# Optimization experiments

Measured on AMD Instinct MI355X. Metric: run time of the kernel, lower is better.

## Reference

```python
import jax, jax.numpy as jnp
import numpy as np

B, T, E, H, D = 256, 77, 1280, 20, 64
SCALE = D ** -0.5
NEG = -1e9


def setup_inputs() -> dict:
    key = jax.random.key(0)
    ks = jax.random.split(key, 32)
    w = lambda k, shape, s=0.02: jax.random.normal(k, shape, dtype=jnp.float32) * s
    causal = jnp.triu(jnp.full((T, T), NEG, dtype=jnp.float32), k=1)
    causal_mask = jnp.broadcast_to(causal[None, None], (B, 1, T, T))
    return {
        'hidden_states': jax.random.normal(ks[0], (B, T, E), dtype=jnp.float32),
        'embeds': jax.random.normal(ks[1], (B, T, E), dtype=jnp.float32),
        'causal_mask': causal_mask,
        'q_w': w(ks[2], (E, E)), 'q_b': w(ks[3], (E,)),
        'k_w': w(ks[4], (E, E)), 'k_b': w(ks[5], (E,)),
        'v_w': w(ks[6], (E, E)), 'v_b': w(ks[7], (E,)),
        'o_w': w(ks[8], (E, E)), 'o_b': w(ks[9], (E,)),
        'ka_w': w(ks[10], (E, E)) * 0.01, 'ka_b': w(ks[11], (E,)) * 0.001,
        'va_w': w(ks[12], (E, E)) * 0.01, 'va_b': w(ks[13], (E,)) * 0.001,
        'zc1_w': w(ks[14], (E, E)), 'zc1_b': w(ks[15], (E,)),
        'zt1_w': w(ks[16], (T, 2 * T)), 'zt1_b': w(ks[17], (T,)),
        'zc2_w': w(ks[18], (E, E)), 'zc2_b': w(ks[19], (E,)),
        'zt2_w': w(ks[20], (T, T)), 'zt2_b': w(ks[21], (T,)),
    }


def _heads(x):
    # (B, S, E) -> (B, H, S, D)
    return x.reshape(B, -1, H, D).transpose(0, 2, 1, 3)


def _attend(q, k, v, mask=None):
    # q,k,v: (B,H,*,D); returns (B,T,E)
    logits = jnp.einsum('bhtd,bhsd->bhts', q, k)
    if mask is not None:
        logits = logits + mask  # mask: (B,1,T,S)
    probs = jax.nn.softmax(logits, axis=-1)  # dropout p=0 in eval
    ctx = jnp.einsum('bhts,bhsd->bhtd', probs, v)
    return ctx.transpose(0, 2, 1, 3).reshape(B, T, E)


def _zipper(x, zc1_w, zc1_b, zt1_w, zt1_b, zc2_w, zc2_b, zt2_w, zt2_b):
    # token/channel mixer: (B, 2T, E) -> (B, T, E)
    x = jax.nn.gelu(x @ zc1_w.T + zc1_b)              # channel: E -> hidden E
    x = jnp.swapaxes(x, 1, 2)                          # (B, E, 2T)
    x = jax.nn.gelu(x @ zt1_w.T + zt1_b)               # tokens: 2T -> T
    x = jnp.swapaxes(x, 1, 2)                          # (B, T, E)
    x = x @ zc2_w.T + zc2_b                            # channel: E -> E
    x = jnp.swapaxes(x, 1, 2) @ zt2_w.T + zt2_b        # tokens: T -> T
    return jnp.swapaxes(x, 1, 2)


def reference(hidden_states, embeds, causal_mask,
              q_w, q_b, k_w, k_b, v_w, v_b, o_w, o_b,
              ka_w, ka_b, va_w, va_b,
              zc1_w, zc1_b, zt1_w, zt1_b, zc2_w, zc2_b, zt2_w, zt2_b):
    q = _heads((hidden_states @ q_w.T + q_b) * SCALE)
    k = _heads(hidden_states @ k_w.T + k_b)
    v = _heads(hidden_states @ v_w.T + v_b)
    attn_output = _attend(q, k, v, causal_mask)  # self-attention pass

    # adapter cross-attention pass (shared query)
    ka = _heads(embeds @ ka_w.T + ka_b)
    va = _heads(embeds @ va_w.T + va_b)
    attn_output_adapter = _attend(q, ka, va, None)

    zipped = _zipper(jnp.concatenate([attn_output_adapter, attn_output], axis=1),
                     zc1_w, zc1_b, zt1_w, zt1_b, zc2_w, zc2_b, zt2_w, zt2_b)
    attn_output = attn_output + zipped
    return attn_output @ o_w.T + o_b
```

## Files before the change

kernel.cpp:

```cpp
#include <hip/hip_runtime.h>
#include <stdint.h>

#define B_    256
#define T_    77
#define E_    1280
#define H_    20
#define T2_   154
#define MTOK  19712
#define MTOK2 39424

typedef float f32x4 __attribute__((ext_vector_type(4)));
typedef short bf16x8 __attribute__((ext_vector_type(8)));

__device__ inline float bf2f(short s) {
    return __uint_as_float(((unsigned)(unsigned short)s) << 16);
}
__device__ inline short f2bf(float f) {
    unsigned u = __float_as_uint(f);
    u += 0x7fff + ((u >> 16) & 1);
    return (short)(u >> 16);
}
__device__ inline float gelu_tanh(float x) {
    float x3 = x * x * x;
    return 0.5f * x * (1.0f + tanhf(0.7978845608028654f * (x + 0.044715f * x3)));
}

__global__ void cast_f32_bf16(const float* __restrict__ in, short* __restrict__ out, int n4) {
    int i = blockIdx.x * blockDim.x + threadIdx.x;
    int stride = gridDim.x * blockDim.x;
    for (; i < n4; i += stride) {
        float4 v = reinterpret_cast<const float4*>(in)[i];
        short4 o;
        o.x = f2bf(v.x); o.y = f2bf(v.y); o.z = f2bf(v.z); o.w = f2bf(v.w);
        reinterpret_cast<short4*>(out)[i] = o;
    }
}

__global__ void cast8_f32_bf16(const float* __restrict__ s0, const float* __restrict__ s1,
                               const float* __restrict__ s2, const float* __restrict__ s3,
                               const float* __restrict__ s4, const float* __restrict__ s5,
                               const float* __restrict__ s6, const float* __restrict__ s7,
                               short* __restrict__ out) {
    const int per = E_ * E_ / 4;
    int i = blockIdx.x * blockDim.x + threadIdx.x;
    int stride = gridDim.x * blockDim.x;
    for (; i < 8 * per; i += stride) {
        int w = i / per, j = i - w * per;
        const float* src = w == 0 ? s0 : w == 1 ? s1 : w == 2 ? s2 : w == 3 ? s3
                         : w == 4 ? s4 : w == 5 ? s5 : w == 6 ? s6 : s7;
        float4 v = reinterpret_cast<const float4*>(src)[j];
        short4 o;
        o.x = f2bf(v.x); o.y = f2bf(v.y); o.z = f2bf(v.z); o.w = f2bf(v.w);
        reinterpret_cast<short4*>(out)[i] = o;
    }
}

__global__ void pad_weight(const float* __restrict__ W, short* __restrict__ Wp,
                           int rows, int cols, int KP) {
    int i = blockIdx.x * 256 + threadIdx.x;
    if (i >= 80 * KP) return;
    int t = i / KP, s = i - t * KP;
    Wp[i] = (t < rows && s < cols) ? f2bf(W[t * cols + s]) : (short)0;
}

#define GEMM_CORE(A_, W_, KDIM, ACC)                                                   \
    const int rsub = lane >> 3;                                                        \
    const int col  = (((lane & 7) ^ rsub) & 7) * 8;                                    \
    const int swz  = (lane & 7) << 3;                                                  \
    for (int kt = 0; kt < (KDIM); kt += 64) {                                          \
        __syncthreads();                                                               \
        _Pragma("unroll")                                                              \
        for (int i = 0; i < 4; ++i) {                                                  \
            int chunk = i * 4 + wave;                                                  \
            int row = chunk * 8 + rsub;                                                \
            const short* ga = (A_) + (arow0 + row) * (KDIM) + kt + col;                \
            const short* gb = (W_) + (brow0 + row) * (KDIM) + kt + col;                \
            __builtin_amdgcn_global_load_lds(                                          \
                (const __attribute__((address_space(1))) unsigned int*)ga,             \
                (__attribute__((address_space(3))) unsigned int*)&Als[chunk * 512],    \
                16, 0, 0);                                                             \
            __builtin_amdgcn_global_load_lds(                                          \
                (const __attribute__((address_space(1))) unsigned int*)gb,             \
                (__attribute__((address_space(3))) unsigned int*)&Bls[chunk * 512],    \
                16, 0, 0);                                                             \
        }                                                                              \
        __syncthreads();                                                               \
        _Pragma("unroll")                                                              \
        for (int kk = 0; kk < 2; ++kk) {                                               \
            bf16x8 af[4], bfr[4];                                                      \
            _Pragma("unroll")                                                          \
            for (int mi = 0; mi < 4; ++mi)                                             \
                af[mi] = *reinterpret_cast<const bf16x8*>(                             \
                    &Als[(((wm + mi * 16 + (lane & 15)) * 64 + kk * 32 +               \
                           (lane >> 4) * 8)) ^ swz]);                                  \
            _Pragma("unroll")                                                          \
            for (int nj = 0; nj < 4; ++nj)                                             \
                bfr[nj] = *reinterpret_cast<const bf16x8*>(                            \
                    &Bls[(((wn + nj * 16 + (lane & 15)) * 64 + kk * 32 +               \
                           (lane >> 4) * 8)) ^ swz]);                                  \
            _Pragma("unroll")                                                          \
            for (int mi = 0; mi < 4; ++mi)                                             \
                _Pragma("unroll")                                                      \
                for (int nj = 0; nj < 4; ++nj)                                         \
                    ACC[mi][nj] = __builtin_amdgcn_mfma_f32_16x16x32_bf16(             \
                        af[mi], bfr[nj], ACC[mi][nj], 0, 0, 0);                        \
        }                                                                              \
    }

template<int EPI>
__global__ void gemm_bt(const short* __restrict__ A, const short* __restrict__ W,
                        const float* __restrict__ bias, void* __restrict__ Cout,
                        int K) {
    const int N = E_;
    const int NBN = E_ / 128;
    __shared__ short Als[128 * 64];
    __shared__ short Bls[128 * 64];
    const int tid  = threadIdx.x;
    const int wave = tid >> 6, lane = tid & 63;

    const int nwg = gridDim.x;
    const int qq = nwg >> 3, rr = nwg & 7;
    const int x = blockIdx.x & 7, ii = blockIdx.x >> 3;
    const int L = (x < rr ? x * (qq + 1) : rr * (qq + 1) + (x - rr) * qq) + ii;
    const int bm = L / NBN, bn = L % NBN;

    const int wm = (wave >> 1) * 64, wn = (wave & 1) * 64;
    f32x4 acc[4][4] = {};
    const long arow0 = (long)bm * 128;
    const long brow0 = (long)bn * 128;

    GEMM_CORE(A, W, K, acc)

#pragma unroll
    for (int mi = 0; mi < 4; ++mi) {
#pragma unroll
        for (int nj = 0; nj < 4; ++nj) {
            int gcol = bn * 128 + wn + nj * 16 + (lane & 15);
            float bv = bias[gcol];
#pragma unroll
            for (int r = 0; r < 4; ++r) {
                long grow = arow0 + wm + mi * 16 + (lane >> 4) * 4 + r;
                float v = acc[mi][nj][r] + bv;
                if (EPI == 2) v = gelu_tanh(v);
                if (EPI == 3) ((float*)Cout)[grow * N + gcol] = v;
                else          ((short*)Cout)[grow * N + gcol] = f2bf(v);
            }
        }
    }
}

template<int NSEG>
__global__ void gemm_proj(const short* __restrict__ A, const short* __restrict__ W,
                          const float* __restrict__ b0, const float* __restrict__ b1,
                          const float* __restrict__ b2,
                          short* __restrict__ o0, short* __restrict__ o1,
                          short* __restrict__ o2, float s0) {
    const int PB = (MTOK / 128) * (E_ / 128);
    __shared__ short Als[128 * 64];
    __shared__ short Bls[128 * 64];
    const int tid  = threadIdx.x;
    const int wave = tid >> 6, lane = tid & 63;

    const int nwg = gridDim.x;
    const int qq = nwg >> 3, rr = nwg & 7;
    const int x = blockIdx.x & 7, ii = blockIdx.x >> 3;
    const int L = (x < rr ? x * (qq + 1) : rr * (qq + 1) + (x - rr) * qq) + ii;
    const int seg = L / PB;
    const int rem = L - seg * PB;
    const int bm = rem / (E_ / 128), bnl = rem % (E_ / 128);

    const int wm = (wave >> 1) * 64, wn = (wave & 1) * 64;
    f32x4 acc[4][4] = {};
    const long arow0 = (long)bm * 128;
    const long brow0 = (long)seg * E_ + bnl * 128;
    const int K = E_;

    GEMM_CORE(A, W, K, acc)

    const float* bias = seg == 0 ? b0 : (seg == 1 ? b1 : b2);
    short* out = seg == 0 ? o0 : (seg == 1 ? o1 : o2);
    const float scl = seg == 0 ? s0 : 1.f;
#pragma unroll
    for (int mi = 0; mi < 4; ++mi) {
#pragma unroll
        for (int nj = 0; nj < 4; ++nj) {
            int gcol = bnl * 128 + wn + nj * 16 + (lane & 15);
            float bv = bias[gcol];
#pragma unroll
            for (int r = 0; r < 4; ++r) {
                long grow = arow0 + wm + mi * 16 + (lane >> 4) * 4 + r;
                out[grow * E_ + gcol] = f2bf((acc[mi][nj][r] + bv) * scl);
            }
        }
    }
}

template<int SIN, int KP, int PS, bool GELU, bool RESID>
__global__ void mixer_mfma(const short* __restrict__ IN, const short* __restrict__ Wp,
                           const float* __restrict__ bias, const short* __restrict__ Cat,
                           short* __restrict__ OUT) {
    __shared__ short lsT[64 * PS];
    const int e0 = blockIdx.x * 64;
    const int b  = blockIdx.y;
    const int tid = threadIdx.x, wave = tid >> 6, lane = tid & 63;

    const int eg = tid & 7;
    const int sl = tid >> 3;
    for (int sb = sl; sb < KP; sb += 32) {
        if (sb < SIN) {
            bf16x8 v = *reinterpret_cast<const bf16x8*>(
                &IN[((long)b * SIN + sb) * E_ + e0 + eg * 8]);
#pragma unroll
            for (int i = 0; i < 8; ++i)
                lsT[(eg * 8 + i) * PS + sb] = v[i];
        } else {
#pragma unroll
            for (int i = 0; i < 8; ++i)
                lsT[(eg * 8 + i) * PS + sb] = 0;
        }
    }
    __syncthreads();

    const int ebase = wave * 16;
    f32x4 acc[5] = {};
#pragma unroll
    for (int ks = 0; ks < KP / 32; ++ks) {
        bf16x8 bfr = *reinterpret_cast<const bf16x8*>(
            &lsT[(ebase + (lane & 15)) * PS + ks * 32 + (lane >> 4) * 8]);
#pragma unroll
        for (int mt = 0; mt < 5; ++mt) {
            bf16x8 af = *reinterpret_cast<const bf16x8*>(
                &Wp[(mt * 16 + (lane & 15)) * KP + ks * 32 + (lane >> 4) * 8]);
            acc[mt] = __builtin_amdgcn_mfma_f32_16x16x32_bf16(af, bfr, acc[mt], 0, 0, 0);
        }
    }

    const int e = e0 + ebase + (lane & 15);
#pragma unroll
    for (int mt = 0; mt < 5; ++mt) {
#pragma unroll
        for (int r = 0; r < 4; ++r) {
            int t = mt * 16 + (lane >> 4) * 4 + r;
            if (t < T_) {
                float v = acc[mt][r] + bias[t];
                if (GELU) v = gelu_tanh(v);
                if (RESID) v += bf2f(Cat[((long)b * T2_ + T_ + t) * E_ + e]);
                OUT[((long)b * T_ + t) * E_ + e] = f2bf(v);
            }
        }
    }
}

#define ASTR 104
__global__ __launch_bounds__(64, 1)
void attn_mfma(const short* __restrict__ Qm,
               const short* __restrict__ Km, const short* __restrict__ Vm,
               const short* __restrict__ KAm, const short* __restrict__ VAm,
               short* __restrict__ Cat) {
    __shared__ short pls[80 * ASTR];
    __shared__ short vt[64 * ASTR];
    const int hh = blockIdx.x;
    const int b = hh / H_, h = hh % H_;
    const int lane = threadIdx.x & 63;
    const int colbase = lane & 15, g = lane >> 4;
    const long base = ((long)b * T_) * E_ + h * 64;

    for (int pass = 0; pass < 2; ++pass) {
        const short* Kp = pass ? KAm : Km;
        const short* Vp = pass ? VAm : Vm;
        const bool causal = (pass == 0);
        const int rowoff = pass ? 0 : T_;

        {
            int4 z = {0, 0, 0, 0};
#pragma unroll
            for (int it = 0; it < 4; ++it) {
                int idx = it * 64 + lane;
                int row = idx >> 2, cb = idx & 3;
                *reinterpret_cast<int4*>(&vt[row * ASTR + 64 + cb * 8]) = z;
            }
#pragma unroll
            for (int it = 0; it < 3; ++it) {
                int idx = it * 64 + lane;
                if (idx < 160) {
                    int row = idx >> 1, cb = idx & 1;
                    *reinterpret_cast<int4*>(&pls[row * ASTR + 80 + cb * 8]) = z;
                }
            }
        }

        {
            const short* vb = Vp + base + (long)lane * E_;
#pragma unroll
            for (int dg = 0; dg < 8; ++dg) {
                bf16x8 v = *reinterpret_cast<const bf16x8*>(vb + dg * 8);
#pragma unroll
                for (int i = 0; i < 8; ++i) vt[(dg * 8 + i) * ASTR + lane] = v[i];
            }
            if (lane < T_ - 64) {
                const short* vb2 = Vp + base + (long)(64 + lane) * E_;
#pragma unroll
                for (int dg = 0; dg < 8; ++dg) {
                    bf16x8 v = *reinterpret_cast<const bf16x8*>(vb2 + dg * 8);
#pragma unroll
                    for (int i = 0; i < 8; ++i) vt[(dg * 8 + i) * ASTR + 64 + lane] = v[i];
                }
            }
        }

        f32x4 sacc[5][5] = {};
#pragma unroll
        for (int kk = 0; kk < 2; ++kk) {
            bf16x8 qf[5];
#pragma unroll
            for (int mi = 0; mi < 5; ++mi) {
                int t = mi * 16 + colbase; t = t > 76 ? 76 : t;
                qf[mi] = *reinterpret_cast<const bf16x8*>(
                    Qm + base + (long)t * E_ + kk * 32 + g * 8);
            }
#pragma unroll
            for (int nj = 0; nj < 5; ++nj) {
                int s = nj * 16 + colbase; s = s > 76 ? 76 : s;
                bf16x8 kf = *reinterpret_cast<const bf16x8*>(
                    Kp + base + (long)s * E_ + kk * 32 + g * 8);
#pragma unroll
                for (int mi = 0; mi < 5; ++mi)
                    sacc[mi][nj] = __builtin_amdgcn_mfma_f32_16x16x32_bf16(
                        qf[mi], kf, sacc[mi][nj], 0, 0, 0);
            }
        }

        float inv[5][4];
#pragma unroll
        for (int mi = 0; mi < 5; ++mi) {
#pragma unroll
            for (int r = 0; r < 4; ++r) {
                int t = mi * 16 + g * 4 + r;
                float mx = -3.0e38f;
#pragma unroll
                for (int nj = 0; nj < 5; ++nj) {
                    int s = nj * 16 + colbase;
                    bool ok = causal ? (s <= t) : (s < T_);
                    if (ok) mx = fmaxf(mx, sacc[mi][nj][r]);
                }
#pragma unroll
                for (int o = 1; o <= 8; o <<= 1) mx = fmaxf(mx, __shfl_xor(mx, o));
                float sum = 0.f;
#pragma unroll
                for (int nj = 0; nj < 5; ++nj) {
                    int s = nj * 16 + colbase;
                    bool ok = causal ? (s <= t) : (s < T_);
                    float pv = ok ? __expf(sacc[mi][nj][r] - mx) : 0.f;
                    sacc[mi][nj][r] = pv;
                    sum += pv;
                }
#pragma unroll
                for (int o = 1; o <= 8; o <<= 1) sum += __shfl_xor(sum, o);
                inv[mi][r] = 1.0f / sum;
            }
        }

#pragma unroll
        for (int mi = 0; mi < 5; ++mi)
#pragma unroll
            for (int nj = 0; nj < 5; ++nj)
#pragma unroll
                for (int r = 0; r < 4; ++r)
                    pls[(mi * 16 + g * 4 + r) * ASTR + nj * 16 + colbase] =
                        f2bf(sacc[mi][nj][r]);

        f32x4 cacc[5][4] = {};
#pragma unroll
        for (int ks = 0; ks < 3; ++ks) {
            bf16x8 pa[5];
#pragma unroll
            for (int mi = 0; mi < 5; ++mi)
                pa[mi] = *reinterpret_cast<const bf16x8*>(
                    &pls[(mi * 16 + colbase) * ASTR + ks * 32 + g * 8]);
#pragma unroll
            for (int nd = 0; nd < 4; ++nd) {
                bf16x8 vf = *reinterpret_cast<const bf16x8*>(
                    &vt[(nd * 16 + colbase) * ASTR + ks * 32 + g * 8]);
#pragma unroll
                for (int mi = 0; mi < 5; ++mi)
                    cacc[mi][nd] = __builtin_amdgcn_mfma_f32_16x16x32_bf16(
                        pa[mi], vf, cacc[mi][nd], 0, 0, 0);
            }
        }

#pragma unroll
        for (int mi = 0; mi < 5; ++mi)
#pragma unroll
            for (int nd = 0; nd < 4; ++nd)
#pragma unroll
                for (int r = 0; r < 4; ++r) {
                    int t = mi * 16 + g * 4 + r;
                    if (t < T_) {
                        float val = cacc[mi][nd][r] * inv[mi][r];
                        Cat[((long)b * T2_ + rowoff + t) * E_ + h * 64 + nd * 16 + colbase] =
                            f2bf(val);
                    }
                }
    }
}

extern "C" void kernel_launch(void* const* d_in, const int* in_sizes, int n_in,
                              void* d_out, int out_size, void* d_ws, size_t ws_size,
                              hipStream_t stream) {
    const float* hidden = (const float*)d_in[0];
    const float* embeds = (const float*)d_in[1];
    const float* q_w  = (const float*)d_in[3];  const float* q_b  = (const float*)d_in[4];
    const float* k_w  = (const float*)d_in[5];  const float* k_b  = (const float*)d_in[6];
    const float* v_w  = (const float*)d_in[7];  const float* v_b  = (const float*)d_in[8];
    const float* o_w  = (const float*)d_in[9];  const float* o_b  = (const float*)d_in[10];
    const float* ka_w = (const float*)d_in[11]; const float* ka_b = (const float*)d_in[12];
    const float* va_w = (const float*)d_in[13]; const float* va_b = (const float*)d_in[14];
    const float* zc1_w = (const float*)d_in[15]; const float* zc1_b = (const float*)d_in[16];
    const float* zt1_w = (const float*)d_in[17]; const float* zt1_b = (const float*)d_in[18];
    const float* zc2_w = (const float*)d_in[19]; const float* zc2_b = (const float*)d_in[20];
    const float* zt2_w = (const float*)d_in[21]; const float* zt2_b = (const float*)d_in[22];

    char* ws = (char*)d_ws;
    const size_t WSZ = (size_t)E_ * E_ * 2;
    const size_t ASZ = (size_t)MTOK * E_ * 2;
    short* Wq  = (short*)(ws + 0 * WSZ);
    short* Wka = (short*)(ws + 3 * WSZ);
    short* Wz1 = (short*)(ws + 5 * WSZ);
    short* Wz2 = (short*)(ws + 6 * WSZ);
    short* Wo  = (short*)(ws + 7 * WSZ);
    char* p = ws + 8 * WSZ;
    short* Ahs  = (short*)p; p += ASZ;
    short* Aemb = (short*)p; p += ASZ;
    short* Qb   = (short*)p; p += ASZ;
    short* Kb   = (short*)p; p += ASZ;
    short* Vb   = (short*)p; p += ASZ;
    short* KAb  = (short*)p; p += ASZ;
    short* VAb  = (short*)p; p += ASZ;
    short* Wz1p = (short*)p; p += 80 * 160 * 2;
    short* Wz2p = (short*)p; p += 80 * 96 * 2;
    short* CAT = Ahs;
    short* Y   = KAb;
    short* X2  = Qb;
    short* X3  = Kb;
    short* S   = Vb;

    if (ws_size < (size_t)(p - ws)) return;

    cast_f32_bf16<<<2048, 256, 0, stream>>>(hidden, Ahs,  MTOK * E_ / 4);
    cast_f32_bf16<<<2048, 256, 0, stream>>>(embeds, Aemb, MTOK * E_ / 4);
    cast8_f32_bf16<<<2048, 256, 0, stream>>>(q_w, k_w, v_w, ka_w, va_w, zc1_w, zc2_w, o_w,
                                             Wq);
    pad_weight<<<(80 * 160 + 255) / 256, 256, 0, stream>>>(zt1_w, Wz1p, 77, 154, 160);
    pad_weight<<<(80 * 96 + 255) / 256, 256, 0, stream>>>(zt2_w, Wz2p, 77, 77, 96);

    const int gQKV  = (MTOK / 128) * (3 * E_ / 128);
    const int gKAVA = (MTOK / 128) * (2 * E_ / 128);
    const int g154  = (MTOK / 128) * (E_ / 128);
    const int g308  = (MTOK2 / 128) * (E_ / 128);
    gemm_proj<3><<<gQKV, 256, 0, stream>>>(Ahs, Wq, q_b, k_b, v_b,
                                           Qb, Kb, Vb, 0.125f);
    gemm_proj<2><<<gKAVA, 256, 0, stream>>>(Aemb, Wka, ka_b, va_b, nullptr,
                                            KAb, VAb, nullptr, 1.f);
    attn_mfma<<<B_ * H_, 64, 0, stream>>>(Qb, Kb, Vb, KAb, VAb, CAT);
    gemm_bt<2><<<g308, 256, 0, stream>>>(CAT, Wz1, zc1_b, Y, E_);
    mixer_mfma<154, 160, 168, true, false><<<dim3(E_ / 64, B_), 256, 0, stream>>>(
        Y, Wz1p, zt1_b, nullptr, X2);
    gemm_bt<0><<<g154, 256, 0, stream>>>(X2, Wz2, zc2_b, X3, E_);
    mixer_mfma<77, 96, 104, false, true><<<dim3(E_ / 64, B_), 256, 0, stream>>>(
        X3, Wz2p, zt2_b, CAT, S);
    gemm_bt<3><<<g154, 256, 0, stream>>>(S, Wo, o_b, (float*)d_out, E_);
}
```

Before: 1.057 ms.

## Replace projection and zc1 GEMMs with 256x256 double-buffered 8-wave GEMM kernel

Adds a new qgemm kernel that uses 256x256 output tiles with 512 threads, double-buffered LDS staging through global_load_lds, and a four-phase schedule that interleaves the next tile's loads with MFMA work under explicit waitcnt and barrier control. It replaces the QKV, adapter KA/VA and the zc1 channel GEMMs, which previously used 128x128 single-buffered tiles. The larger tiles are meant to raise data reuse per byte loaded and to hide global memory latency behind compute. In exchange the kernel needs more LDS and registers per block, and the hand-written vmcnt counts make it fragile.

```diff
diff --git a/kernel.cpp b/kernel.cpp
--- a/kernel.cpp
+++ b/kernel.cpp
@@ -61,6 +61,168 @@
     if (i >= 80 * KP) return;
     int t = i / KP, s = i - t * KP;
     Wp[i] = (t < rows && s < cols) ? f2bf(W[t * cols + s]) : (short)0;
+}
+
+template<int NSEG, int EPI>
+__global__ __launch_bounds__(512, 2)
+void qgemm(const short* __restrict__ A, const short* __restrict__ W,
+           const float* __restrict__ b0, const float* __restrict__ b1,
+           const float* __restrict__ b2,
+           short* __restrict__ o0, short* __restrict__ o1, short* __restrict__ o2,
+           float s0) {
+    const int K = E_;
+    const int NT = K / 64;
+    __shared__ short As[2 * 2 * 8192];
+    __shared__ short Bs[2 * 2 * 8192];
+    const int tid = threadIdx.x;
+    const int wave = tid >> 6, lane = tid & 63;
+    const int wr = wave >> 2, wc = wave & 3;
+
+    const int nwg = gridDim.x;
+    const int qq = nwg >> 3, rr = nwg & 7;
+    const int x = blockIdx.x & 7, ii = blockIdx.x >> 3;
+    const int L = (x < rr ? x * (qq + 1) : rr * (qq + 1) + (x - rr) * qq) + ii;
+    const int PB = nwg / NSEG;
+    const int seg = L / PB;
+    const int rem = L - seg * PB;
+    const int bm = rem / 5, bnl = rem % 5;
+
+    const long arow0 = (long)bm * 256;
+    const long brow0 = (long)seg * E_ + bnl * 256;
+
+    const int rsub = lane >> 3;
+    const int colswz = (((lane & 7) ^ rsub) & 7) * 8;
+    const int swz = (lane & 7) << 3;
+
+    f32x4 acc[8][4] = {};
+
+    auto STAGE_A = [&](int par, int half, int kt) {
+#pragma unroll
+        for (int i = 0; i < 2; ++i) {
+            int chunk = i * 8 + wave;
+            int row = chunk * 8 + rsub;
+            const short* ga = A + (arow0 + half * 128 + row) * K + kt * 64 + colswz;
+            __builtin_amdgcn_global_load_lds(
+                (const __attribute__((address_space(1))) unsigned int*)ga,
+                (__attribute__((address_space(3))) unsigned int*)
+                    &As[par * 16384 + half * 8192 + chunk * 512], 16, 0, 0);
+        }
+    };
+    auto STAGE_B = [&](int par, int half, int kt) {
+#pragma unroll
+        for (int i = 0; i < 2; ++i) {
+            int chunk = i * 8 + wave;
+            int row = chunk * 8 + rsub;
+            const short* gb = W + (brow0 + half * 128 + row) * K + kt * 64 + colswz;
+            __builtin_amdgcn_global_load_lds(
+                (const __attribute__((address_space(1))) unsigned int*)gb,
+                (__attribute__((address_space(3))) unsigned int*)
+                    &Bs[par * 16384 + half * 8192 + chunk * 512], 16, 0, 0);
+        }
+    };
+
+    bf16x8 Afr[4][2], Bfr[2][2];
+    auto LDA = [&](int par, int hm) {
+#pragma unroll
+        for (int mi = 0; mi < 4; ++mi)
+#pragma unroll
+            for (int kk = 0; kk < 2; ++kk)
+                Afr[mi][kk] = *reinterpret_cast<const bf16x8*>(
+                    &As[par * 16384 + hm * 8192 +
+                        (((wr * 64 + mi * 16 + (lane & 15)) * 64 + kk * 32 +
+                          (lane >> 4) * 8) ^ swz)]);
+    };
+    auto LDB = [&](int par, int hn) {
+#pragma unroll
+        for (int nj = 0; nj < 2; ++nj)
+#pragma unroll
+            for (int kk = 0; kk < 2; ++kk)
+                Bfr[nj][kk] = *reinterpret_cast<const bf16x8*>(
+                    &Bs[par * 16384 + hn * 8192 +
+                        (((wc * 32 + nj * 16 + (lane & 15)) * 64 + kk * 32 +
+                          (lane >> 4) * 8) ^ swz)]);
+    };
+    auto MFMA16 = [&](int hm, int hn) {
+        __builtin_amdgcn_s_setprio(1);
+#pragma unroll
+        for (int mi = 0; mi < 4; ++mi)
+#pragma unroll
+            for (int nj = 0; nj < 2; ++nj)
+#pragma unroll
+                for (int kk = 0; kk < 2; ++kk)
+                    acc[hm * 4 + mi][hn * 2 + nj] =
+                        __builtin_amdgcn_mfma_f32_16x16x32_bf16(
+                            Afr[mi][kk], Bfr[nj][kk], acc[hm * 4 + mi][hn * 2 + nj],
+                            0, 0, 0);
+        __builtin_amdgcn_s_setprio(0);
+    };
+
+    STAGE_A(0, 0, 0); STAGE_B(0, 0, 0); STAGE_B(0, 1, 0); STAGE_A(0, 1, 0);
+
+    for (int t = 0; t < NT - 1; ++t) {
+        const int par = t & 1, nxt = par ^ 1;
+        asm volatile("s_waitcnt vmcnt(4)" ::: "memory");
+        __builtin_amdgcn_s_barrier(); __builtin_amdgcn_sched_barrier(0);
+        LDA(par, 0); LDB(par, 0);
+        STAGE_A(nxt, 0, t + 1);
+        MFMA16(0, 0);
+        asm volatile("s_waitcnt vmcnt(4)" ::: "memory");
+        __builtin_amdgcn_s_barrier(); __builtin_amdgcn_sched_barrier(0);
+        LDB(par, 1);
+        STAGE_B(nxt, 0, t + 1);
+        MFMA16(0, 1);
+        asm volatile("s_waitcnt vmcnt(4)" ::: "memory");
+        __builtin_amdgcn_s_barrier(); __builtin_amdgcn_sched_barrier(0);
+        LDA(par, 1); LDB(par, 0);
+        STAGE_B(nxt, 1, t + 1);
+        MFMA16(1, 0);
+        __builtin_amdgcn_s_barrier(); __builtin_amdgcn_sched_barrier(0);
+        LDB(par, 1);
+        STAGE_A(nxt, 1, t + 1);
+        MFMA16(1, 1);
+    }
+    {
+        const int par = (NT - 1) & 1;
+        asm volatile("s_waitcnt vmcnt(4)" ::: "memory");
+        __builtin_amdgcn_s_barrier(); __builtin_amdgcn_sched_barrier(0);
+        LDA(par, 0); LDB(par, 0);
+        MFMA16(0, 0);
+        asm volatile("s_waitcnt vmcnt(2)" ::: "memory");
+        __builtin_amdgcn_s_barrier(); __builtin_amdgcn_sched_barrier(0);
+        LDB(par, 1);
+        MFMA16(0, 1);
+        asm volatile("s_waitcnt vmcnt(0)" ::: "memory");
+        __builtin_amdgcn_s_barrier(); __builtin_amdgcn_sched_barrier(0);
+        LDA(par, 1); LDB(par, 0);
+        MFMA16(1, 0);
+        __builtin_amdgcn_s_barrier(); __builtin_amdgcn_sched_barrier(0);
+        LDB(par, 1);
+        MFMA16(1, 1);
+    }
+
+    const float* bias = seg == 0 ? b0 : (seg == 1 ? b1 : b2);
+    short* out = seg == 0 ? o0 : (seg == 1 ? o1 : o2);
+    const float scl = (EPI == 0 && seg == 0) ? s0 : 1.f;
+#pragma unroll
+    for (int hm = 0; hm < 2; ++hm)
+#pragma unroll
+        for (int mi = 0; mi < 4; ++mi)
+#pragma unroll
+            for (int hn = 0; hn < 2; ++hn)
+#pragma unroll
+                for (int nj = 0; nj < 2; ++nj) {
+                    int ncol = bnl * 256 + hn * 128 + wc * 32 + nj * 16 + (lane & 15);
+                    float bv = bias[ncol];
+#pragma unroll
+                    for (int r = 0; r < 4; ++r) {
+                        long grow = arow0 + hm * 128 + wr * 64 + mi * 16 +
+                                    (lane >> 4) * 4 + r;
+                        float v = acc[hm * 4 + mi][hn * 2 + nj][r] + bv;
+                        if (EPI == 2) v = gelu_tanh(v);
+                        else v *= scl;
+                        out[grow * E_ + ncol] = f2bf(v);
+                    }
+                }
 }
 
 #define GEMM_CORE(A_, W_, KDIM, ACC)                                                   \
@@ -141,55 +303,8 @@
             for (int r = 0; r < 4; ++r) {
                 long grow = arow0 + wm + mi * 16 + (lane >> 4) * 4 + r;
                 float v = acc[mi][nj][r] + bv;
-                if (EPI == 2) v = gelu_tanh(v);
                 if (EPI == 3) ((float*)Cout)[grow * N + gcol] = v;
                 else          ((short*)Cout)[grow * N + gcol] = f2bf(v);
-            }
-        }
-    }
-}
-
-template<int NSEG>
-__global__ void gemm_proj(const short* __restrict__ A, const short* __restrict__ W,
-                          const float* __restrict__ b0, const float* __restrict__ b1,
-                          const float* __restrict__ b2,
-                          short* __restrict__ o0, short* __restrict__ o1,
-                          short* __restrict__ o2, float s0) {
-    const int PB = (MTOK / 128) * (E_ / 128);
-    __shared__ short Als[128 * 64];
-    __shared__ short Bls[128 * 64];
-    const int tid  = threadIdx.x;
-    const int wave = tid >> 6, lane = tid & 63;
-
-    const int nwg = gridDim.x;
-    const int qq = nwg >> 3, rr = nwg & 7;
-    const int x = blockIdx.x & 7, ii = blockIdx.x >> 3;
-    const int L = (x < rr ? x * (qq + 1) : rr * (qq + 1) + (x - rr) * qq) + ii;
-    const int seg = L / PB;
-    const int rem = L - seg * PB;
-    const int bm = rem / (E_ / 128), bnl = rem % (E_ / 128);
-
-    const int wm = (wave >> 1) * 64, wn = (wave & 1) * 64;
-    f32x4 acc[4][4] = {};
-    const long arow0 = (long)bm * 128;
-    const long brow0 = (long)seg * E_ + bnl * 128;
-    const int K = E_;
-
-    GEMM_CORE(A, W, K, acc)
-
-    const float* bias = seg == 0 ? b0 : (seg == 1 ? b1 : b2);
-    short* out = seg == 0 ? o0 : (seg == 1 ? o1 : o2);
-    const float scl = seg == 0 ? s0 : 1.f;
-#pragma unroll
-    for (int mi = 0; mi < 4; ++mi) {
-#pragma unroll
-        for (int nj = 0; nj < 4; ++nj) {
-            int gcol = bnl * 128 + wn + nj * 16 + (lane & 15);
-            float bv = bias[gcol];
-#pragma unroll
-            for (int r = 0; r < 4; ++r) {
-                long grow = arow0 + wm + mi * 16 + (lane >> 4) * 4 + r;
-                out[grow * E_ + gcol] = f2bf((acc[mi][nj][r] + bv) * scl);
             }
         }
     }
@@ -453,16 +568,17 @@
     pad_weight<<<(80 * 160 + 255) / 256, 256, 0, stream>>>(zt1_w, Wz1p, 77, 154, 160);
     pad_weight<<<(80 * 96 + 255) / 256, 256, 0, stream>>>(zt2_w, Wz2p, 77, 77, 96);
 
-    const int gQKV  = (MTOK / 128) * (3 * E_ / 128);
-    const int gKAVA = (MTOK / 128) * (2 * E_ / 128);
+    const int gQKV  = (MTOK / 256) * (3 * E_ / 256);
+    const int gKAVA = (MTOK / 256) * (2 * E_ / 256);
+    const int gZC1  = (MTOK2 / 256) * (E_ / 256);
     const int g154  = (MTOK / 128) * (E_ / 128);
-    const int g308  = (MTOK2 / 128) * (E_ / 128);
-    gemm_proj<3><<<gQKV, 256, 0, stream>>>(Ahs, Wq, q_b, k_b, v_b,
-                                           Qb, Kb, Vb, 0.125f);
-    gemm_proj<2><<<gKAVA, 256, 0, stream>>>(Aemb, Wka, ka_b, va_b, nullptr,
-                                            KAb, VAb, nullptr, 1.f);
+    qgemm<3, 0><<<gQKV, 512, 0, stream>>>(Ahs, Wq, q_b, k_b, v_b,
+                                          Qb, Kb, Vb, 0.125f);
+    qgemm<2, 0><<<gKAVA, 512, 0, stream>>>(Aemb, Wka, ka_b, va_b, va_b,
+                                           KAb, VAb, VAb, 1.f);
     attn_mfma<<<B_ * H_, 64, 0, stream>>>(Qb, Kb, Vb, KAb, VAb, CAT);
-    gemm_bt<2><<<g308, 256, 0, stream>>>(CAT, Wz1, zc1_b, Y, E_);
+    qgemm<1, 2><<<gZC1, 512, 0, stream>>>(CAT, Wz1, zc1_b, zc1_b, zc1_b,
+                                          Y, Y, Y, 1.f);
     mixer_mfma<154, 160, 168, true, false><<<dim3(E_ / 64, B_), 256, 0, stream>>>(
         Y, Wz1p, zt1_b, nullptr, X2);
     gemm_bt<0><<<g154, 256, 0, stream>>>(X2, Wz2, zc2_b, X3, E_);
```

New measurement: 1.154 ms. 9.1% more time.
